# Performance work log

Measured on AMD Instinct MI355X. Metric: run time of the kernel, lower is better.

## Reference

```python
import jax, jax.numpy as jnp
from jax import lax
import numpy as np

KERNEL_SIZE = 24

def setup_inputs() -> dict:
    key = jax.random.key(0)
    k1, k2, k3, k4 = jax.random.split(key, 4)
    B, C, T = 16, 1024, 3000
    x = jax.random.normal(k1, (B, C, T, 1), dtype=jnp.float32)
    alpha = jax.random.uniform(k2, (C,), dtype=jnp.float32)   # in (0,1): decaying kernels
    beta = jax.random.normal(k3, (C,), dtype=jnp.float32)
    theta = jax.random.uniform(k4, (C,), dtype=jnp.float32)
    return {"x": x, "alpha": alpha, "beta": beta, "theta": theta}

def _cos_approx(x):
    x2 = x * x
    return 1.0 - 0.5 * x2 + (x2 * x2) * (1.0 / 24.0)

def reference(x, alpha, beta, theta):
    B, C, T, _ = x.shape
    K = KERNEL_SIZE
    t_idx = jnp.arange(K, dtype=x.dtype)                      # (K,)
    log_alpha = jnp.log(jnp.clip(alpha, 1e-6))                # (C,)
    decay = jnp.exp(log_alpha[:, None] * t_idx)               # (C,K)
    phase = _cos_approx(theta[:, None] * t_idx)               # (C,K)
    kernel = (beta[:, None] * decay * phase)[:, None, :]      # (C,1,K) depthwise
    # causal depthwise conv1d: left-pad K-1 (torch F.conv1d and lax conv are both correlations)
    y = lax.conv_general_dilated(
        x[..., 0], kernel,
        window_strides=(1,), padding=[(K - 1, 0)],
        dimension_numbers=("NCH", "OIH", "NCH"),
        feature_group_count=C,
    )                                                         # (B,C,T)
    return y[..., None]                                       # (B,C,T,1)
```

## Files before the change

### kernel.cpp

```cpp
#include <hip/hip_runtime.h>


#define KSZ   24
#define T_LEN 3000
#define C_CH  1024
#define B_N   16
#define OPT   4
#define TPB   256
#define TILE  (TPB * OPT)

typedef float f32x4 __attribute__((ext_vector_type(4)));

__device__ __forceinline__ float cos_approx(float v) {
    float v2 = v * v;
    return 1.0f - 0.5f * v2 + (v2 * v2) * (1.0f / 24.0f);
}

__global__ __launch_bounds__(TPB) void ssm4d_conv(
        const float* __restrict__ x,
        const float* __restrict__ alpha,
        const float* __restrict__ beta,
        const float* __restrict__ theta,
        float* __restrict__ y) {
    const int row   = blockIdx.y;
    const int c     = row & (C_CH - 1);
    const long base = (long)row * T_LEN;

    __shared__ float ws[KSZ];
    if (threadIdx.x < KSZ) {
        const int k = (KSZ - 1) - threadIdx.x;
        const float a   = fmaxf(alpha[c], 1e-6f);
        const float dec = expf(logf(a) * (float)k);
        ws[threadIdx.x] = beta[c] * dec * cos_approx(theta[c] * (float)k);
    }
    __syncthreads();

    const int t = blockIdx.x * TILE + threadIdx.x * OPT;
    if (t < T_LEN) {
        float wr[KSZ];
#pragma unroll
        for (int d = 0; d < KSZ; ++d) wr[d] = ws[d];

        float win[KSZ + OPT];
        if (t >= KSZ) {
            const float4* xp = (const float4*)(x + base + t - KSZ);
#pragma unroll
            for (int q = 0; q < (KSZ + OPT) / 4; ++q) {
                float4 v = xp[q];
                win[4 * q + 0] = v.x; win[4 * q + 1] = v.y;
                win[4 * q + 2] = v.z; win[4 * q + 3] = v.w;
            }
        } else {
#pragma unroll
            for (int p = 0; p < KSZ + OPT; ++p) {
                const int idx = t - KSZ + p;
                win[p] = (idx >= 0) ? x[base + idx] : 0.0f;
            }
        }

        float acc[OPT];
#pragma unroll
        for (int m = 0; m < OPT; ++m) acc[m] = 0.0f;
#pragma unroll
        for (int d = 0; d < KSZ; ++d) {
#pragma unroll
            for (int m = 0; m < OPT; ++m)
                acc[m] = fmaf(wr[d], win[KSZ + m - d], acc[m]);
        }

        f32x4 out = { acc[0], acc[1], acc[2], acc[3] };
        __builtin_nontemporal_store(out, (f32x4*)(y + base + t));
    }
}

extern "C" void kernel_launch(void* const* d_in, const int* in_sizes, int n_in,
                              void* d_out, int out_size, void* d_ws, size_t ws_size,
                              hipStream_t stream) {
    const float* x     = (const float*)d_in[0];
    const float* alpha = (const float*)d_in[1];
    const float* beta  = (const float*)d_in[2];
    const float* theta = (const float*)d_in[3];
    float* y = (float*)d_out;

    dim3 grid((T_LEN + TILE - 1) / TILE, B_N * C_CH);
    ssm4d_conv<<<grid, TPB, 0, stream>>>(x, alpha, beta, theta, y);
}
```

Baseline: 341.1 us.

## Stage whole row in padded LDS, one block per row

Each block now handles an entire (b,c) row: it loads the full 3000-sample row into padded shared memory once, then computes three output tiles from LDS instead of re-reading overlapping 28-float windows from global memory. The grid shrinks to one block per row, which removes the halo reloads and lets the filter taps be computed once per row instead of once per tile. The nontemporal store becomes a normal store. In exchange it uses about 12KB of LDS per block, which can limit occupancy, and it adds a barrier between the load and compute phases.

```diff
diff --git a/kernel.cpp b/kernel.cpp
--- a/kernel.cpp
+++ b/kernel.cpp
@@ -5,9 +5,14 @@
 #define T_LEN 3000
 #define C_CH  1024
 #define B_N   16
+#define TPB   256
 #define OPT   4
-#define TPB   256
 #define TILE  (TPB * OPT)
+#define CHK   (T_LEN / 4)
+#define PADC  (KSZ / 4)
+#define LMAX  (CHK + PADC - 1)
+#define PPOS(L) ((L) + ((L) >> 3))
+#define LDSN  (PPOS(LMAX) + 1)
 
 typedef float f32x4 __attribute__((ext_vector_type(4)));
 
@@ -22,54 +27,60 @@
         const float* __restrict__ beta,
         const float* __restrict__ theta,
         float* __restrict__ y) {
-    const int row   = blockIdx.y;
+    const int row   = blockIdx.x;
     const int c     = row & (C_CH - 1);
     const long base = (long)row * T_LEN;
+    const int tid   = threadIdx.x;
 
     __shared__ float ws[KSZ];
-    if (threadIdx.x < KSZ) {
-        const int k = (KSZ - 1) - threadIdx.x;
+    __shared__ f32x4 lds[LDSN];
+
+    const f32x4* xp = (const f32x4*)(x + base);
+    const int c0 = tid, c1 = tid + TPB, c2 = tid + 2 * TPB;
+    f32x4 a0 = xp[c0];
+    f32x4 a1 = xp[c1];
+    f32x4 a2 = (c2 < CHK) ? xp[c2] : (f32x4){0.f, 0.f, 0.f, 0.f};
+
+    if (tid < KSZ) {
+        const int k = (KSZ - 1) - tid;
         const float a   = fmaxf(alpha[c], 1e-6f);
         const float dec = expf(logf(a) * (float)k);
-        ws[threadIdx.x] = beta[c] * dec * cos_approx(theta[c] * (float)k);
+        ws[tid] = beta[c] * dec * cos_approx(theta[c] * (float)k);
     }
+    if (tid < PADC) lds[tid] = (f32x4){0.f, 0.f, 0.f, 0.f};
+
+    lds[PPOS(c0 + PADC)] = a0;
+    lds[PPOS(c1 + PADC)] = a1;
+    if (c2 < CHK) lds[PPOS(c2 + PADC)] = a2;
     __syncthreads();
 
-    const int t = blockIdx.x * TILE + threadIdx.x * OPT;
-    if (t < T_LEN) {
-        float wr[KSZ];
+    float wr[KSZ];
 #pragma unroll
-        for (int d = 0; d < KSZ; ++d) wr[d] = ws[d];
+    for (int d = 0; d < KSZ; ++d) wr[d] = ws[d];
 
-        float win[KSZ + OPT];
-        if (t >= KSZ) {
-            const float4* xp = (const float4*)(x + base + t - KSZ);
+#pragma unroll
+    for (int s = 0; s < 3; ++s) {
+        const int t = s * TILE + tid * OPT;
+        if (t < T_LEN) {
+            float win[KSZ + OPT];
+            const int L0 = s * (TILE / 4) + tid;
 #pragma unroll
             for (int q = 0; q < (KSZ + OPT) / 4; ++q) {
-                float4 v = xp[q];
+                f32x4 v = lds[PPOS(L0 + q)];
                 win[4 * q + 0] = v.x; win[4 * q + 1] = v.y;
                 win[4 * q + 2] = v.z; win[4 * q + 3] = v.w;
             }
-        } else {
+            float acc[OPT];
 #pragma unroll
-            for (int p = 0; p < KSZ + OPT; ++p) {
-                const int idx = t - KSZ + p;
-                win[p] = (idx >= 0) ? x[base + idx] : 0.0f;
+            for (int m = 0; m < OPT; ++m) acc[m] = 0.0f;
+#pragma unroll
+            for (int d = 0; d < KSZ; ++d) {
+#pragma unroll
+                for (int m = 0; m < OPT; ++m)
+                    acc[m] = fmaf(wr[d], win[KSZ + m - d], acc[m]);
             }
+            *(float4*)(y + base + t) = make_float4(acc[0], acc[1], acc[2], acc[3]);
         }
-
-        float acc[OPT];
-#pragma unroll
-        for (int m = 0; m < OPT; ++m) acc[m] = 0.0f;
-#pragma unroll
-        for (int d = 0; d < KSZ; ++d) {
-#pragma unroll
-            for (int m = 0; m < OPT; ++m)
-                acc[m] = fmaf(wr[d], win[KSZ + m - d], acc[m]);
-        }
-
-        f32x4 out = { acc[0], acc[1], acc[2], acc[3] };
-        __builtin_nontemporal_store(out, (f32x4*)(y + base + t));
     }
 }
 
@@ -82,6 +93,5 @@
     const float* theta = (const float*)d_in[3];
     float* y = (float*)d_out;
 
-    dim3 grid((T_LEN + TILE - 1) / TILE, B_N * C_CH);
-    ssm4d_conv<<<grid, TPB, 0, stream>>>(x, alpha, beta, theta, y);
+    ssm4d_conv<<<B_N * C_CH, TPB, 0, stream>>>(x, alpha, beta, theta, y);
 }
```

Result: faster. 328.1 us (-3.8%).
